# Optimization experiments

Measured on AMD Instinct MI355X. Metric: run time of the kernel, lower is better.

The kernel has to match this reference:

```python
import jax, jax.numpy as jnp
import numpy as np

D_MODEL = 1024
NUM_HEADS = 16
DEPTH = D_MODEL // NUM_HEADS  # 64
BATCH, SEQ = 4, 2048


def setup_inputs() -> dict:
    key = jax.random.key(0)
    ks = jax.random.split(key, 9)
    s = 1.0 / np.sqrt(D_MODEL)
    x = jax.random.normal(ks[0], (BATCH, SEQ, D_MODEL), dtype=jnp.float32)
    # Per-head Dense weights stacked on a leading head axis [H, d_model, depth]
    Wq = jax.random.normal(ks[1], (NUM_HEADS, D_MODEL, DEPTH), dtype=jnp.float32) * s
    Wk = jax.random.normal(ks[2], (NUM_HEADS, D_MODEL, DEPTH), dtype=jnp.float32) * s
    Wv = jax.random.normal(ks[3], (NUM_HEADS, D_MODEL, DEPTH), dtype=jnp.float32) * s
    bq = jnp.zeros((NUM_HEADS, DEPTH), dtype=jnp.float32)
    bk = jnp.zeros((NUM_HEADS, DEPTH), dtype=jnp.float32)
    bv = jnp.zeros((NUM_HEADS, DEPTH), dtype=jnp.float32)
    Wo = jax.random.normal(ks[4], (D_MODEL, D_MODEL), dtype=jnp.float32) * s
    bo = jnp.zeros((D_MODEL,), dtype=jnp.float32)
    return {"x": x, "Wq": Wq, "bq": bq, "Wk": Wk, "bk": bk,
            "Wv": Wv, "bv": bv, "Wo": Wo, "bo": bo}


def reference(x, Wq, bq, Wk, bk, Wv, bv, Wo, bo):
    # Batched equivalent of the per-head loop: project, attend, concat heads.
    q = jnp.einsum('bsd,hde->bhse', x, Wq) + bq[:, None, :]  # [B,H,S,depth]
    k = jnp.einsum('bsd,hde->bhse', x, Wk) + bk[:, None, :]
    v = jnp.einsum('bsd,hde->bhse', x, Wv) + bv[:, None, :]
    scale = 1.0 / jnp.sqrt(jnp.asarray(DEPTH, dtype=x.dtype))
    scores = jnp.einsum('bhse,bhte->bhst', q, k) * scale      # [B,H,S,S]
    weights = jax.nn.softmax(scores, axis=-1)
    heads = jnp.einsum('bhst,bhte->bhse', weights, v)         # [B,H,S,depth]
    # concat head outputs along last axis in head order (tf.concat axis=-1)
    multi = jnp.transpose(heads, (0, 2, 1, 3)).reshape(x.shape[0], x.shape[1], D_MODEL)
    return multi @ Wo + bo
```

## Files before the change

kernel.cpp:

```cpp
#include <hip/hip_runtime.h>
#include <hip/hip_bf16.h>

#define BATCH 4
#define SEQ   2048
#define DM    1024
#define NH    16
#define DEPTH 64
#define ROWS  (BATCH*SEQ)
#define NQKV  (3*DM)
#define BH    (BATCH*NH)

typedef __attribute__((ext_vector_type(8))) short bf16x8;
typedef __attribute__((ext_vector_type(4))) float f32x4;
typedef unsigned short u16;
typedef unsigned int   u32;

__device__ __forceinline__ u16 f2bf(float f) {
    union { float f; unsigned u; } v; v.f = f;
    unsigned r = v.u + 0x7fff + ((v.u >> 16) & 1);
    return (u16)(r >> 16);
}

__device__ __forceinline__ u32 pk2bf(float a, float b) {
#if __has_builtin(__builtin_amdgcn_cvt_pk_bf16_f32)
    typedef __attribute__((ext_vector_type(2))) __bf16 v2bf;
    union { v2bf v; u32 u; } u_;
    u_.v = __builtin_amdgcn_cvt_pk_bf16_f32(a, b);
    return u_.u;
#else
    return (u32)f2bf(a) | ((u32)f2bf(b) << 16);
#endif
}

__device__ __forceinline__ void g2l16(void* lds, const void* g) {
    __builtin_amdgcn_global_load_lds((const __attribute__((address_space(1))) void*)g,
                                     (__attribute__((address_space(3))) void*)lds, 16, 0, 0);
}

__device__ __forceinline__ bf16x8 frag8(const u16* tile, int row, int gl) {
    return *(const bf16x8*)(tile + row * 64 + ((gl ^ (row & 7)) * 8));
}

__global__ __launch_bounds__(256) void k_prep(const float* __restrict__ x,
                                              const float* __restrict__ Wq, const float* __restrict__ Wk,
                                              const float* __restrict__ Wv, const float* __restrict__ Wo,
                                              u16* __restrict__ xb, u16* __restrict__ BT, u16* __restrict__ WoT) {
    __shared__ u16 T[64][65];
    int tid = threadIdx.x;
    int bx = blockIdx.x;
    if (bx < 2048) {
        int i = bx * 4096 + tid * 4;
        for (int l = 0; l < 4; ++l) {
            float4 v = *(const float4*)(x + i + l * 1024);
            ushort4 o; o.x = f2bf(v.x); o.y = f2bf(v.y); o.z = f2bf(v.z); o.w = f2bf(v.w);
            *(ushort4*)(xb + i + l * 1024) = o;
        }
        return;
    }
    if (bx < 2816) {
        int q = bx - 2048;
        int kt = q & 15, mh = q >> 4, m = mh >> 4, h = mh & 15;
        const float* W = (m == 0) ? Wq : (m == 1) ? Wk : Wv;
        const float* src = W + ((size_t)h * 1024 + kt * 64) * 64;
        int e = tid & 63, r0 = tid >> 6;
        for (int i = 0; i < 16; ++i) { int r = i * 4 + r0; T[r][e] = f2bf(src[r * 64 + e]); }
        __syncthreads();
        int kk = tid & 63, e0 = tid >> 6;
        u16* dst = BT + ((size_t)m * 1024 + h * 64) * 1024 + kt * 64;
        for (int i = 0; i < 16; ++i) { int ee = i * 4 + e0; dst[ee * 1024 + kk] = T[kk][ee]; }
        return;
    }
    {
        int q = bx - 2816;
        int kt = q & 15, nt = q >> 4;
        const float* src = Wo + (size_t)kt * 64 * 1024 + nt * 64;
        int c = tid & 63, r0 = tid >> 6;
        for (int i = 0; i < 16; ++i) { int r = i * 4 + r0; T[r][c] = f2bf(src[r * 1024 + c]); }
        __syncthreads();
        int kk = tid & 63, e0 = tid >> 6;
        u16* dst = WoT + (size_t)nt * 64 * 1024 + kt * 64;
        for (int i = 0; i < 16; ++i) { int ee = i * 4 + e0; dst[ee * 1024 + kk] = T[kk][ee]; }
    }
}

__global__ __launch_bounds__(256) void k_gemm_qk(const u16* __restrict__ A, const u16* __restrict__ BT,
                                                 const float* __restrict__ bq, const float* __restrict__ bk,
                                                 u16* __restrict__ Q, u16* __restrict__ K) {
    __shared__ u16 Al[128 * 64];
    __shared__ u16 Bl[128 * 64];
    int tid = threadIdx.x;
    int wave = tid >> 6, lane = tid & 63, ln = lane & 15, quad = lane >> 4;
    int row0 = blockIdx.y * 128;
    int col0 = blockIdx.x * 128;
    int moff = (wave >> 1) * 64, noff = (wave & 1) * 64;
    f32x4 acc[4][4] = {};

    for (int k0 = 0; k0 < 1024; k0 += 64) {
        for (int l = 0; l < 4; ++l) {
            int idx = tid + l * 256, r = idx >> 3, gs = ((idx & 7) ^ (r & 7)) * 8;
            g2l16(&Al[idx * 8], A  + (row0 + r) * 1024 + k0 + gs);
            g2l16(&Bl[idx * 8], BT + (col0 + r) * 1024 + k0 + gs);
        }
        __syncthreads();
        for (int kk = 0; kk < 2; ++kk) {
            bf16x8 a[4], b[4];
            for (int i = 0; i < 4; ++i) a[i] = frag8(Al, moff + i * 16 + ln, kk * 4 + quad);
            for (int j = 0; j < 4; ++j) b[j] = frag8(Bl, noff + j * 16 + ln, kk * 4 + quad);
            for (int i = 0; i < 4; ++i)
                for (int j = 0; j < 4; ++j)
                    acc[i][j] = __builtin_amdgcn_mfma_f32_16x16x32_bf16(a[i], b[j], acc[i][j], 0, 0, 0);
        }
        __syncthreads();
    }

    const float QSCALE = 0.125f * 1.4426950408889634f;
    for (int j = 0; j < 4; ++j) {
        int c = col0 + noff + j * 16 + ln;
        int m = c >> 10, h = (c >> 6) & 15, e = c & 63;
        const float* bias = (m == 0) ? bq : bk;
        float bval = bias[h * 64 + e];
        for (int i = 0; i < 4; ++i) {
            for (int r = 0; r < 4; ++r) {
                int rowg = row0 + moff + i * 16 + quad * 4 + r;
                int b_ = rowg >> 11, s = rowg & 2047;
                int bh = b_ * 16 + h;
                float v = acc[i][j][r] + bval;
                if (m == 0) Q[(bh * 2048 + s) * 64 + e] = f2bf(v * QSCALE);
                else        K[(bh * 2048 + s) * 64 + e] = f2bf(v);
            }
        }
    }
}

__global__ __launch_bounds__(256) void k_gemm_vt(const u16* __restrict__ A, const u16* __restrict__ BT,
                                                 const float* __restrict__ bv, u16* __restrict__ VT) {
    __shared__ u16 Al[128 * 64];
    __shared__ u16 Bl[128 * 64];
    int tid = threadIdx.x;
    int wave = tid >> 6, lane = tid & 63, ln = lane & 15, quad = lane >> 4;
    int row0 = blockIdx.y * 128;
    int col0 = blockIdx.x * 128;
    int moff = (wave >> 1) * 64, noff = (wave & 1) * 64;
    f32x4 acc[4][4] = {};

    for (int k0 = 0; k0 < 1024; k0 += 64) {
        for (int l = 0; l < 4; ++l) {
            int idx = tid + l * 256, r = idx >> 3, gs = ((idx & 7) ^ (r & 7)) * 8;
            g2l16(&Al[idx * 8], A  + (row0 + r) * 1024 + k0 + gs);
            g2l16(&Bl[idx * 8], BT + (col0 + r) * 1024 + k0 + gs);
        }
        __syncthreads();
        for (int kk = 0; kk < 2; ++kk) {
            bf16x8 a[4], b[4];
            for (int i = 0; i < 4; ++i) a[i] = frag8(Al, moff + i * 16 + ln, kk * 4 + quad);
            for (int j = 0; j < 4; ++j) b[j] = frag8(Bl, noff + j * 16 + ln, kk * 4 + quad);
            for (int i = 0; i < 4; ++i)
                for (int j = 0; j < 4; ++j)
                    acc[i][j] = __builtin_amdgcn_mfma_f32_16x16x32_bf16(a[i], b[j], acc[i][j], 0, 0, 0);
        }
        __syncthreads();
    }

    for (int j = 0; j < 4; ++j) {
        int c = col0 + noff + j * 16 + ln;
        int b_ = c >> 11, s = c & 2047;
        for (int i = 0; i < 4; ++i) {
            for (int r = 0; r < 4; ++r) {
                int ii = row0 + moff + i * 16 + quad * 4 + r;
                float v = acc[i][j][r] + bv[ii];
                VT[((size_t)b_ * 1024 + ii) * 2048 + s] = f2bf(v);
            }
        }
    }
}

__global__ __launch_bounds__(256) void k_attn(const u16* __restrict__ Q, const u16* __restrict__ K,
                                              const u16* __restrict__ VT, u16* __restrict__ A2) {
    __shared__ u16 Ql[128 * 64];
    __shared__ u16 Kl[64 * 64];
    __shared__ u16 Vl[64 * 64];
    int tid = threadIdx.x;
    int wave = tid >> 6, lane = tid & 63, ln = lane & 15, quad = lane >> 4;
    int bh = blockIdx.y;
    int m0 = blockIdx.x * 128;
    const u16* Qb = Q + (size_t)bh * 2048 * 64;
    const u16* Kb = K + (size_t)bh * 2048 * 64;
    const u16* Vb = VT + (size_t)bh * 64 * 2048;

    int rA = tid >> 3,  gA = ((tid & 7) ^ (rA & 7)) * 8;
    int idxB = tid + 256;
    int rB = idxB >> 3, gB = ((idxB & 7) ^ (rB & 7)) * 8;
    const u16* kgA = Kb + rA * 64 + gA;
    const u16* kgB = Kb + rB * 64 + gB;
    const u16* vgA = Vb + rA * 2048 + gA;
    const u16* vgB = Vb + rB * 2048 + gB;

    for (int l = 0; l < 4; ++l) {
        int idx = tid + l * 256, r = idx >> 3, gs = ((idx & 7) ^ (r & 7)) * 8;
        g2l16(&Ql[idx * 8], Qb + (m0 + r) * 64 + gs);
    }
    g2l16(&Kl[tid * 8],  kgA);
    g2l16(&Kl[idxB * 8], kgB);
    g2l16(&Vl[tid * 8],  vgA);
    g2l16(&Vl[idxB * 8], vgB);
    __syncthreads();
    bf16x8 qb[2][2];
    for (int s = 0; s < 2; ++s)
        for (int kk = 0; kk < 2; ++kk)
            qb[s][kk] = frag8(Ql, wave * 32 + s * 16 + ln, kk * 4 + quad);

    bf16x8 ones;
    for (int i = 0; i < 8; ++i) ones[i] = (short)0x3F80;

    f32x4 oacc[2][4] = {};
    f32x4 lacc[2] = {};

    for (int t = 0; t < 32; ++t) {
        f32x4 sc[2][4] = {};
        for (int kk = 0; kk < 2; ++kk) {
            bf16x8 kf[4];
            for (int j = 0; j < 4; ++j) kf[j] = frag8(Kl, j * 16 + ln, kk * 4 + quad);
            for (int s = 0; s < 2; ++s)
                for (int j = 0; j < 4; ++j)
                    sc[s][j] = __builtin_amdgcn_mfma_f32_16x16x32_bf16(kf[j], qb[s][kk], sc[s][j], 0, 0, 0);
        }

        for (int s = 0; s < 2; ++s) {
            int prow = wave * 32 + s * 16 + ln;
            char* pbase = (char*)Ql + prow * 128 + (quad & 1) * 8;
            for (int j = 0; j < 4; ++j) {
                float p0 = __builtin_amdgcn_exp2f(sc[s][j][0]);
                float p1 = __builtin_amdgcn_exp2f(sc[s][j][1]);
                float p2 = __builtin_amdgcn_exp2f(sc[s][j][2]);
                float p3 = __builtin_amdgcn_exp2f(sc[s][j][3]);
                uint2 w; w.x = pk2bf(p0, p1); w.y = pk2bf(p2, p3);
                int pg = (j * 2 + (quad >> 1)) ^ (ln & 7);
                *(uint2*)(pbase + pg * 16) = w;
            }
        }

        for (int kk = 0; kk < 2; ++kk) {
            bf16x8 ap0 = frag8(Ql, wave * 32 + ln,      kk * 4 + quad);
            bf16x8 ap1 = frag8(Ql, wave * 32 + 16 + ln, kk * 4 + quad);
            for (int et = 0; et < 4; ++et) {
                bf16x8 bv_ = frag8(Vl, et * 16 + ln, kk * 4 + quad);
                oacc[0][et] = __builtin_amdgcn_mfma_f32_16x16x32_bf16(ap0, bv_, oacc[0][et], 0, 0, 0);
                oacc[1][et] = __builtin_amdgcn_mfma_f32_16x16x32_bf16(ap1, bv_, oacc[1][et], 0, 0, 0);
            }
            lacc[0] = __builtin_amdgcn_mfma_f32_16x16x32_bf16(ap0, ones, lacc[0], 0, 0, 0);
            lacc[1] = __builtin_amdgcn_mfma_f32_16x16x32_bf16(ap1, ones, lacc[1], 0, 0, 0);
        }
        __syncthreads();
        if (t < 31) {
            g2l16(&Kl[tid * 8],  kgA + (t + 1) * 4096);
            g2l16(&Kl[idxB * 8], kgB + (t + 1) * 4096);
            g2l16(&Vl[tid * 8],  vgA + (t + 1) * 64);
            g2l16(&Vl[idxB * 8], vgB + (t + 1) * 64);
        }
        __syncthreads();
    }

    int b_ = bh >> 4, h = bh & 15;
    for (int s = 0; s < 2; ++s) {
        for (int r = 0; r < 4; ++r) {
            float ir = 1.0f / lacc[s][r];
            int rowg = b_ * 2048 + m0 + wave * 32 + s * 16 + quad * 4 + r;
            for (int et = 0; et < 4; ++et)
                A2[rowg * 1024 + h * 64 + et * 16 + ln] = f2bf(oacc[s][et][r] * ir);
        }
    }
}

__global__ __launch_bounds__(256) void k_gemm_out(const u16* __restrict__ A, const u16* __restrict__ BT,
                                                  const float* __restrict__ bo, float* __restrict__ out) {
    __shared__ u16 Al[128 * 64];
    __shared__ u16 Bl[128 * 64];
    int tid = threadIdx.x;
    int wave = tid >> 6, lane = tid & 63, ln = lane & 15, quad = lane >> 4;
    int row0 = blockIdx.y * 128;
    int col0 = blockIdx.x * 128;
    int moff = (wave >> 1) * 64, noff = (wave & 1) * 64;
    f32x4 acc[4][4] = {};

    for (int k0 = 0; k0 < 1024; k0 += 64) {
        for (int l = 0; l < 4; ++l) {
            int idx = tid + l * 256, r = idx >> 3, gs = ((idx & 7) ^ (r & 7)) * 8;
            g2l16(&Al[idx * 8], A  + (row0 + r) * 1024 + k0 + gs);
            g2l16(&Bl[idx * 8], BT + (col0 + r) * 1024 + k0 + gs);
        }
        __syncthreads();
        for (int kk = 0; kk < 2; ++kk) {
            bf16x8 a[4], b[4];
            for (int i = 0; i < 4; ++i) a[i] = frag8(Al, moff + i * 16 + ln, kk * 4 + quad);
            for (int j = 0; j < 4; ++j) b[j] = frag8(Bl, noff + j * 16 + ln, kk * 4 + quad);
            for (int i = 0; i < 4; ++i)
                for (int j = 0; j < 4; ++j)
                    acc[i][j] = __builtin_amdgcn_mfma_f32_16x16x32_bf16(a[i], b[j], acc[i][j], 0, 0, 0);
        }
        __syncthreads();
    }

    for (int j = 0; j < 4; ++j) {
        int c = col0 + noff + j * 16 + ln;
        float bias = bo[c];
        for (int i = 0; i < 4; ++i)
            for (int r = 0; r < 4; ++r) {
                int rowg = row0 + moff + i * 16 + quad * 4 + r;
                out[rowg * 1024 + c] = acc[i][j][r] + bias;
            }
    }
}

extern "C" void kernel_launch(void* const* d_in, const int* in_sizes, int n_in,
                              void* d_out, int out_size, void* d_ws, size_t ws_size,
                              hipStream_t stream) {
    const float* x  = (const float*)d_in[0];
    const float* Wq = (const float*)d_in[1];
    const float* bq = (const float*)d_in[2];
    const float* Wk = (const float*)d_in[3];
    const float* bk = (const float*)d_in[4];
    const float* Wv = (const float*)d_in[5];
    const float* bv = (const float*)d_in[6];
    const float* Wo = (const float*)d_in[7];
    const float* bo = (const float*)d_in[8];
    float* out = (float*)d_out;

    char* ws = (char*)d_ws;
    u16* xb    = (u16*)ws; ws += (size_t)ROWS * DM * 2;
    u16* WqkvT = (u16*)ws; ws += (size_t)NQKV * DM * 2;
    u16* WoT   = (u16*)ws; ws += (size_t)DM * DM * 2;
    u16* Qb    = (u16*)ws; ws += (size_t)BH * SEQ * DEPTH * 2;
    u16* Kb    = (u16*)ws; ws += (size_t)BH * SEQ * DEPTH * 2;
    u16* VTb   = (u16*)ws; ws += (size_t)BH * SEQ * DEPTH * 2;
    u16* A2    = (u16*)ws; ws += (size_t)ROWS * DM * 2;

    k_prep     <<<dim3(3072),   dim3(256), 0, stream>>>(x, Wq, Wk, Wv, Wo, xb, WqkvT, WoT);
    k_gemm_qk  <<<dim3(16, 64), dim3(256), 0, stream>>>(xb, WqkvT, bq, bk, Qb, Kb);
    k_gemm_vt  <<<dim3(64, 8),  dim3(256), 0, stream>>>(WqkvT + 2048 * 1024, xb, bv, VTb);
    k_attn     <<<dim3(16, 64), dim3(256), 0, stream>>>(Qb, Kb, VTb, A2);
    k_gemm_out <<<dim3(8, 64),  dim3(256), 0, stream>>>(A2, WoT, bo, out);
}
```

Baseline: 301.2 us.

## Use 32x32 MFMA in attention with 2-wave blocks and merge QK/VT GEMMs

The attention kernel now uses the 32x32x16 bf16 MFMA with two waves per block, each wave covering 64 query rows. Row sums are computed with VALU adds and a cross-half shuffle instead of an extra MFMA against a ones vector. The separate QK and VT projection GEMMs are merged into one launch with a block-index split, removing a kernel boundary and filling the GPU better. The exchange is higher register pressure per wave and fewer threads per block for staging K/V tiles into LDS.

```diff
diff --git a/kernel.cpp b/kernel.cpp
--- a/kernel.cpp
+++ b/kernel.cpp
@@ -12,6 +12,7 @@
 
 typedef __attribute__((ext_vector_type(8))) short bf16x8;
 typedef __attribute__((ext_vector_type(4))) float f32x4;
+typedef __attribute__((ext_vector_type(16))) float f32x16;
 typedef unsigned short u16;
 typedef unsigned int   u32;
 
@@ -39,6 +40,10 @@
 
 __device__ __forceinline__ bf16x8 frag8(const u16* tile, int row, int gl) {
     return *(const bf16x8*)(tile + row * 64 + ((gl ^ (row & 7)) * 8));
+}
+
+__device__ __forceinline__ f32x16 mfma32(bf16x8 a, bf16x8 b, f32x16 c) {
+    return __builtin_amdgcn_mfma_f32_32x32x16_bf16(a, b, c, 0, 0, 0);
 }
 
 __global__ __launch_bounds__(256) void k_prep(const float* __restrict__ x,
@@ -83,192 +88,177 @@
     }
 }
 
-__global__ __launch_bounds__(256) void k_gemm_qk(const u16* __restrict__ A, const u16* __restrict__ BT,
-                                                 const float* __restrict__ bq, const float* __restrict__ bk,
-                                                 u16* __restrict__ Q, u16* __restrict__ K) {
+__global__ __launch_bounds__(256) void k_gemm_qkv(const u16* __restrict__ xb, const u16* __restrict__ Wt,
+                                                  const float* __restrict__ bq, const float* __restrict__ bk,
+                                                  const float* __restrict__ bv,
+                                                  u16* __restrict__ Q, u16* __restrict__ K, u16* __restrict__ VT) {
     __shared__ u16 Al[128 * 64];
     __shared__ u16 Bl[128 * 64];
     int tid = threadIdx.x;
     int wave = tid >> 6, lane = tid & 63, ln = lane & 15, quad = lane >> 4;
-    int row0 = blockIdx.y * 128;
-    int col0 = blockIdx.x * 128;
+    int b = blockIdx.x;
+    bool isvt = (b >= 1024);
+    int row0, col0;
+    const u16 *Am, *Bm;
+    if (!isvt) {
+        col0 = (b & 15) * 128; row0 = (b >> 4) * 128;
+        Am = xb + (size_t)row0 * 1024; Bm = Wt + (size_t)col0 * 1024;
+    } else {
+        int b2 = b - 1024;
+        col0 = (b2 & 63) * 128; row0 = (b2 >> 6) * 128;
+        Am = Wt + (size_t)2048 * 1024 + (size_t)row0 * 1024; Bm = xb + (size_t)col0 * 1024;
+    }
     int moff = (wave >> 1) * 64, noff = (wave & 1) * 64;
     f32x4 acc[4][4] = {};
 
     for (int k0 = 0; k0 < 1024; k0 += 64) {
         for (int l = 0; l < 4; ++l) {
             int idx = tid + l * 256, r = idx >> 3, gs = ((idx & 7) ^ (r & 7)) * 8;
-            g2l16(&Al[idx * 8], A  + (row0 + r) * 1024 + k0 + gs);
-            g2l16(&Bl[idx * 8], BT + (col0 + r) * 1024 + k0 + gs);
+            g2l16(&Al[idx * 8], Am + r * 1024 + k0 + gs);
+            g2l16(&Bl[idx * 8], Bm + r * 1024 + k0 + gs);
         }
         __syncthreads();
         for (int kk = 0; kk < 2; ++kk) {
-            bf16x8 a[4], b[4];
-            for (int i = 0; i < 4; ++i) a[i] = frag8(Al, moff + i * 16 + ln, kk * 4 + quad);
-            for (int j = 0; j < 4; ++j) b[j] = frag8(Bl, noff + j * 16 + ln, kk * 4 + quad);
+            bf16x8 a[4], bb[4];
+            for (int i = 0; i < 4; ++i) a[i]  = frag8(Al, moff + i * 16 + ln, kk * 4 + quad);
+            for (int j = 0; j < 4; ++j) bb[j] = frag8(Bl, noff + j * 16 + ln, kk * 4 + quad);
             for (int i = 0; i < 4; ++i)
                 for (int j = 0; j < 4; ++j)
-                    acc[i][j] = __builtin_amdgcn_mfma_f32_16x16x32_bf16(a[i], b[j], acc[i][j], 0, 0, 0);
-        }
-        __syncthreads();
-    }
-
-    const float QSCALE = 0.125f * 1.4426950408889634f;
-    for (int j = 0; j < 4; ++j) {
-        int c = col0 + noff + j * 16 + ln;
-        int m = c >> 10, h = (c >> 6) & 15, e = c & 63;
-        const float* bias = (m == 0) ? bq : bk;
-        float bval = bias[h * 64 + e];
-        for (int i = 0; i < 4; ++i) {
-            for (int r = 0; r < 4; ++r) {
-                int rowg = row0 + moff + i * 16 + quad * 4 + r;
-                int b_ = rowg >> 11, s = rowg & 2047;
-                int bh = b_ * 16 + h;
-                float v = acc[i][j][r] + bval;
-                if (m == 0) Q[(bh * 2048 + s) * 64 + e] = f2bf(v * QSCALE);
-                else        K[(bh * 2048 + s) * 64 + e] = f2bf(v);
-            }
-        }
-    }
-}
-
-__global__ __launch_bounds__(256) void k_gemm_vt(const u16* __restrict__ A, const u16* __restrict__ BT,
-                                                 const float* __restrict__ bv, u16* __restrict__ VT) {
-    __shared__ u16 Al[128 * 64];
-    __shared__ u16 Bl[128 * 64];
-    int tid = threadIdx.x;
-    int wave = tid >> 6, lane = tid & 63, ln = lane & 15, quad = lane >> 4;
-    int row0 = blockIdx.y * 128;
-    int col0 = blockIdx.x * 128;
-    int moff = (wave >> 1) * 64, noff = (wave & 1) * 64;
-    f32x4 acc[4][4] = {};
-
-    for (int k0 = 0; k0 < 1024; k0 += 64) {
-        for (int l = 0; l < 4; ++l) {
-            int idx = tid + l * 256, r = idx >> 3, gs = ((idx & 7) ^ (r & 7)) * 8;
-            g2l16(&Al[idx * 8], A  + (row0 + r) * 1024 + k0 + gs);
-            g2l16(&Bl[idx * 8], BT + (col0 + r) * 1024 + k0 + gs);
-        }
-        __syncthreads();
-        for (int kk = 0; kk < 2; ++kk) {
-            bf16x8 a[4], b[4];
-            for (int i = 0; i < 4; ++i) a[i] = frag8(Al, moff + i * 16 + ln, kk * 4 + quad);
-            for (int j = 0; j < 4; ++j) b[j] = frag8(Bl, noff + j * 16 + ln, kk * 4 + quad);
+                    acc[i][j] = __builtin_amdgcn_mfma_f32_16x16x32_bf16(a[i], bb[j], acc[i][j], 0, 0, 0);
+        }
+        __syncthreads();
+    }
+
+    if (!isvt) {
+        const float QSCALE = 0.125f * 1.4426950408889634f;
+        for (int j = 0; j < 4; ++j) {
+            int c = col0 + noff + j * 16 + ln;
+            int m = c >> 10, h = (c >> 6) & 15, e = c & 63;
+            const float* bias = (m == 0) ? bq : bk;
+            float bval = bias[h * 64 + e];
             for (int i = 0; i < 4; ++i)
-                for (int j = 0; j < 4; ++j)
-                    acc[i][j] = __builtin_amdgcn_mfma_f32_16x16x32_bf16(a[i], b[j], acc[i][j], 0, 0, 0);
-        }
-        __syncthreads();
-    }
-
-    for (int j = 0; j < 4; ++j) {
-        int c = col0 + noff + j * 16 + ln;
-        int b_ = c >> 11, s = c & 2047;
-        for (int i = 0; i < 4; ++i) {
-            for (int r = 0; r < 4; ++r) {
-                int ii = row0 + moff + i * 16 + quad * 4 + r;
-                float v = acc[i][j][r] + bv[ii];
-                VT[((size_t)b_ * 1024 + ii) * 2048 + s] = f2bf(v);
-            }
-        }
-    }
-}
-
-__global__ __launch_bounds__(256) void k_attn(const u16* __restrict__ Q, const u16* __restrict__ K,
-                                              const u16* __restrict__ VT, u16* __restrict__ A2) {
+                for (int r = 0; r < 4; ++r) {
+                    int rowg = row0 + moff + i * 16 + quad * 4 + r;
+                    int b_ = rowg >> 11, s = rowg & 2047;
+                    int bh = b_ * 16 + h;
+                    float v = acc[i][j][r] + bval;
+                    if (m == 0) Q[(bh * 2048 + s) * 64 + e] = f2bf(v * QSCALE);
+                    else        K[(bh * 2048 + s) * 64 + e] = f2bf(v);
+                }
+        }
+    } else {
+        for (int j = 0; j < 4; ++j) {
+            int c = col0 + noff + j * 16 + ln;
+            int b_ = c >> 11, s = c & 2047;
+            for (int i = 0; i < 4; ++i)
+                for (int r = 0; r < 4; ++r) {
+                    int ii = row0 + moff + i * 16 + quad * 4 + r;
+                    float v = acc[i][j][r] + bv[ii];
+                    VT[((size_t)b_ * 1024 + ii) * 2048 + s] = f2bf(v);
+                }
+        }
+    }
+}
+
+__global__ __launch_bounds__(128, 2) void k_attn(const u16* __restrict__ Q, const u16* __restrict__ K,
+                                                 const u16* __restrict__ VT, u16* __restrict__ A2) {
     __shared__ u16 Ql[128 * 64];
     __shared__ u16 Kl[64 * 64];
     __shared__ u16 Vl[64 * 64];
+    __shared__ float linv[128];
     int tid = threadIdx.x;
-    int wave = tid >> 6, lane = tid & 63, ln = lane & 15, quad = lane >> 4;
+    int wave = tid >> 6, lane = tid & 63, l31 = lane & 31, h = lane >> 5;
     int bh = blockIdx.y;
     int m0 = blockIdx.x * 128;
     const u16* Qb = Q + (size_t)bh * 2048 * 64;
     const u16* Kb = K + (size_t)bh * 2048 * 64;
     const u16* Vb = VT + (size_t)bh * 64 * 2048;
 
-    int rA = tid >> 3,  gA = ((tid & 7) ^ (rA & 7)) * 8;
-    int idxB = tid + 256;
-    int rB = idxB >> 3, gB = ((idxB & 7) ^ (rB & 7)) * 8;
-    const u16* kgA = Kb + rA * 64 + gA;
-    const u16* kgB = Kb + rB * 64 + gB;
-    const u16* vgA = Vb + rA * 2048 + gA;
-    const u16* vgB = Vb + rB * 2048 + gB;
-
+    const u16* kp[4]; const u16* vp[4]; int dsti[4];
     for (int l = 0; l < 4; ++l) {
-        int idx = tid + l * 256, r = idx >> 3, gs = ((idx & 7) ^ (r & 7)) * 8;
+        int idx = tid + l * 128, r = idx >> 3, gs = ((idx & 7) ^ (r & 7)) * 8;
+        dsti[l] = idx * 8;
+        kp[l] = Kb + r * 64 + gs;
+        vp[l] = Vb + r * 2048 + gs;
+    }
+    for (int l = 0; l < 8; ++l) {
+        int idx = tid + l * 128, r = idx >> 3, gs = ((idx & 7) ^ (r & 7)) * 8;
         g2l16(&Ql[idx * 8], Qb + (m0 + r) * 64 + gs);
     }
-    g2l16(&Kl[tid * 8],  kgA);
-    g2l16(&Kl[idxB * 8], kgB);
-    g2l16(&Vl[tid * 8],  vgA);
-    g2l16(&Vl[idxB * 8], vgB);
+    for (int l = 0; l < 4; ++l) { g2l16(&Kl[dsti[l]], kp[l]); g2l16(&Vl[dsti[l]], vp[l]); }
     __syncthreads();
-    bf16x8 qb[2][2];
-    for (int s = 0; s < 2; ++s)
-        for (int kk = 0; kk < 2; ++kk)
-            qb[s][kk] = frag8(Ql, wave * 32 + s * 16 + ln, kk * 4 + quad);
-
-    bf16x8 ones;
-    for (int i = 0; i < 8; ++i) ones[i] = (short)0x3F80;
-
-    f32x4 oacc[2][4] = {};
-    f32x4 lacc[2] = {};
+
+    bf16x8 qb[2][4];
+    for (int qt = 0; qt < 2; ++qt)
+        for (int s = 0; s < 4; ++s)
+            qb[qt][s] = frag8(Ql, wave * 64 + qt * 32 + l31, 2 * s + h);
+
+    f32x16 oacc[2][2] = {};
+    float lsum[2] = {0.f, 0.f};
 
     for (int t = 0; t < 32; ++t) {
-        f32x4 sc[2][4] = {};
-        for (int kk = 0; kk < 2; ++kk) {
-            bf16x8 kf[4];
-            for (int j = 0; j < 4; ++j) kf[j] = frag8(Kl, j * 16 + ln, kk * 4 + quad);
-            for (int s = 0; s < 2; ++s)
-                for (int j = 0; j < 4; ++j)
-                    sc[s][j] = __builtin_amdgcn_mfma_f32_16x16x32_bf16(kf[j], qb[s][kk], sc[s][j], 0, 0, 0);
-        }
-
-        for (int s = 0; s < 2; ++s) {
-            int prow = wave * 32 + s * 16 + ln;
-            char* pbase = (char*)Ql + prow * 128 + (quad & 1) * 8;
-            for (int j = 0; j < 4; ++j) {
-                float p0 = __builtin_amdgcn_exp2f(sc[s][j][0]);
-                float p1 = __builtin_amdgcn_exp2f(sc[s][j][1]);
-                float p2 = __builtin_amdgcn_exp2f(sc[s][j][2]);
-                float p3 = __builtin_amdgcn_exp2f(sc[s][j][3]);
-                uint2 w; w.x = pk2bf(p0, p1); w.y = pk2bf(p2, p3);
-                int pg = (j * 2 + (quad >> 1)) ^ (ln & 7);
-                *(uint2*)(pbase + pg * 16) = w;
+        f32x16 sc[2][2] = {};
+        for (int s = 0; s < 4; ++s) {
+            bf16x8 kf0 = frag8(Kl, l31,      2 * s + h);
+            bf16x8 kf1 = frag8(Kl, 32 + l31, 2 * s + h);
+            for (int qt = 0; qt < 2; ++qt) {
+                sc[0][qt] = mfma32(kf0, qb[qt][s], sc[0][qt]);
+                sc[1][qt] = mfma32(kf1, qb[qt][s], sc[1][qt]);
             }
         }
 
-        for (int kk = 0; kk < 2; ++kk) {
-            bf16x8 ap0 = frag8(Ql, wave * 32 + ln,      kk * 4 + quad);
-            bf16x8 ap1 = frag8(Ql, wave * 32 + 16 + ln, kk * 4 + quad);
-            for (int et = 0; et < 4; ++et) {
-                bf16x8 bv_ = frag8(Vl, et * 16 + ln, kk * 4 + quad);
-                oacc[0][et] = __builtin_amdgcn_mfma_f32_16x16x32_bf16(ap0, bv_, oacc[0][et], 0, 0, 0);
-                oacc[1][et] = __builtin_amdgcn_mfma_f32_16x16x32_bf16(ap1, bv_, oacc[1][et], 0, 0, 0);
+        for (int qt = 0; qt < 2; ++qt) {
+            int prow = wave * 64 + qt * 32 + l31;
+            int rm = prow & 7;
+            char* pbase = (char*)Ql + prow * 128 + 8 * h;
+            float sq = 0.f;
+            for (int kt = 0; kt < 2; ++kt)
+                for (int g = 0; g < 4; ++g) {
+                    float p0 = __builtin_amdgcn_exp2f(sc[kt][qt][g * 4 + 0]);
+                    float p1 = __builtin_amdgcn_exp2f(sc[kt][qt][g * 4 + 1]);
+                    float p2 = __builtin_amdgcn_exp2f(sc[kt][qt][g * 4 + 2]);
+                    float p3 = __builtin_amdgcn_exp2f(sc[kt][qt][g * 4 + 3]);
+                    sq += (p0 + p1) + (p2 + p3);
+                    uint2 w; w.x = pk2bf(p0, p1); w.y = pk2bf(p2, p3);
+                    *(uint2*)(pbase + ((kt * 4 + g) ^ rm) * 16) = w;
+                }
+            lsum[qt] += sq;
+        }
+
+        for (int s = 0; s < 4; ++s) {
+            bf16x8 ap0 = frag8(Ql, wave * 64 + l31,      2 * s + h);
+            bf16x8 ap1 = frag8(Ql, wave * 64 + 32 + l31, 2 * s + h);
+            bf16x8 bv0 = frag8(Vl, l31,      2 * s + h);
+            bf16x8 bv1 = frag8(Vl, 32 + l31, 2 * s + h);
+            oacc[0][0] = mfma32(ap0, bv0, oacc[0][0]);
+            oacc[0][1] = mfma32(ap0, bv1, oacc[0][1]);
+            oacc[1][0] = mfma32(ap1, bv0, oacc[1][0]);
+            oacc[1][1] = mfma32(ap1, bv1, oacc[1][1]);
+        }
+        __syncthreads();
+        if (t < 31) {
+            for (int l = 0; l < 4; ++l) {
+                g2l16(&Kl[dsti[l]], kp[l] + (t + 1) * 4096);
+                g2l16(&Vl[dsti[l]], vp[l] + (t + 1) * 64);
             }
-            lacc[0] = __builtin_amdgcn_mfma_f32_16x16x32_bf16(ap0, ones, lacc[0], 0, 0, 0);
-            lacc[1] = __builtin_amdgcn_mfma_f32_16x16x32_bf16(ap1, ones, lacc[1], 0, 0, 0);
-        }
-        __syncthreads();
-        if (t < 31) {
-            g2l16(&Kl[tid * 8],  kgA + (t + 1) * 4096);
-            g2l16(&Kl[idxB * 8], kgB + (t + 1) * 4096);
-            g2l16(&Vl[tid * 8],  vgA + (t + 1) * 64);
-            g2l16(&Vl[idxB * 8], vgB + (t + 1) * 64);
-        }
-        __syncthreads();
-    }
-
-    int b_ = bh >> 4, h = bh & 15;
-    for (int s = 0; s < 2; ++s) {
-        for (int r = 0; r < 4; ++r) {
-            float ir = 1.0f / lacc[s][r];
-            int rowg = b_ * 2048 + m0 + wave * 32 + s * 16 + quad * 4 + r;
-            for (int et = 0; et < 4; ++et)
-                A2[rowg * 1024 + h * 64 + et * 16 + ln] = f2bf(oacc[s][et][r] * ir);
-        }
-    }
+        }
+        __syncthreads();
+    }
+
+    for (int qt = 0; qt < 2; ++qt) {
+        float l2 = lsum[qt] + __shfl_xor(lsum[qt], 32);
+        linv[wave * 64 + qt * 32 + l31] = 1.0f / l2;
+    }
+    int b_ = bh >> 4, hh = bh & 15;
+    for (int qt = 0; qt < 2; ++qt)
+        for (int g = 0; g < 4; ++g) {
+            f32x4 iv = *(f32x4*)&linv[wave * 64 + qt * 32 + 8 * g + 4 * h];
+            for (int dt = 0; dt < 2; ++dt)
+                for (int r = 0; r < 4; ++r) {
+                    int row = b_ * 2048 + m0 + wave * 64 + qt * 32 + 8 * g + 4 * h + r;
+                    A2[row * 1024 + hh * 64 + dt * 32 + l31] = f2bf(oacc[qt][dt][g * 4 + r] * iv[r]);
+                }
+        }
 }
 
 __global__ __launch_bounds__(256) void k_gemm_out(const u16* __restrict__ A, const u16* __restrict__ BT,
@@ -335,8 +325,7 @@
     u16* A2    = (u16*)ws; ws += (size_t)ROWS * DM * 2;
 
     k_prep     <<<dim3(3072),   dim3(256), 0, stream>>>(x, Wq, Wk, Wv, Wo, xb, WqkvT, WoT);
-    k_gemm_qk  <<<dim3(16, 64), dim3(256), 0, stream>>>(xb, WqkvT, bq, bk, Qb, Kb);
-    k_gemm_vt  <<<dim3(64, 8),  dim3(256), 0, stream>>>(WqkvT + 2048 * 1024, xb, bv, VTb);
-    k_attn     <<<dim3(16, 64), dim3(256), 0, stream>>>(Qb, Kb, VTb, A2);
+    k_gemm_qkv <<<dim3(1536),   dim3(256), 0, stream>>>(xb, WqkvT, bq, bk, bv, Qb, Kb, VTb);
+    k_attn     <<<dim3(16, 64), dim3(128), 0, stream>>>(Qb, Kb, VTb, A2);
     k_gemm_out <<<dim3(8, 64),  dim3(256), 0, stream>>>(A2, WoT, bo, out);
 }
```

Result: faster. 288.0 us (-4.4%).
